# Performance work log

Measured on AMD Instinct MI355X. Metric: run time of the kernel, lower is better.

The kernel has to match this reference:

```python
import jax, jax.numpy as jnp
import numpy as np

EPS = 1e-12  # torch F.normalize eps


def _unfold(x, k, pad, stride):
    # torch F.unfold: [B,C,H,W] -> [B, C*k*k, L], channel-major then kernel (i,j)
    B, C, H, W = x.shape
    xp = jnp.pad(x, ((0, 0), (0, 0), (pad, pad), (pad, pad)))
    Ho = (H + 2 * pad - k) // stride + 1
    Wo = (W + 2 * pad - k) // stride + 1
    patches = [xp[:, :, i:i + stride * (Ho - 1) + 1:stride, j:j + stride * (Wo - 1) + 1:stride]
               for i in range(k) for j in range(k)]
    p = jnp.stack(patches, axis=2)  # [B, C, k*k, Ho, Wo]
    return p.reshape(B, C * k * k, Ho * Wo)


def _fold(t, out_hw, k, pad, stride):
    # torch F.fold: [B, C*k*k, L] -> [B, C, H, W] with overlap-add
    B, Ckk, L = t.shape
    C = Ckk // (k * k)
    H, W = out_hw
    Ho = (H + 2 * pad - k) // stride + 1
    Wo = (W + 2 * pad - k) // stride + 1
    t = t.reshape(B, C, k, k, Ho, Wo)
    out = jnp.zeros((B, C, H + 2 * pad, W + 2 * pad), t.dtype)
    for i in range(k):
        for j in range(k):
            out = out.at[:, :, i:i + stride * (Ho - 1) + 1:stride,
                         j:j + stride * (Wo - 1) + 1:stride].add(t[:, :, i, j])
    return out[:, :, pad:pad + H, pad:pad + W]


def setup_inputs() -> dict:
    key = jax.random.key(0)
    ks = jax.random.split(key, 5)
    B, C3, H3 = 4, 256, 48
    return {
        'dh_img_lv3': jax.random.normal(ks[0], (B, C3, H3, H3), jnp.float32),
        'dh_ref_lv3': jax.random.normal(ks[1], (B, C3, H3, H3), jnp.float32),
        'cl_ref_lv1': jax.random.normal(ks[2], (B, 64, H3 * 4, H3 * 4), jnp.float32),
        'cl_ref_lv2': jax.random.normal(ks[3], (B, 128, H3 * 2, H3 * 2), jnp.float32),
        'cl_ref_lv3': jax.random.normal(ks[4], (B, C3, H3, H3), jnp.float32),
    }


def reference(dh_img_lv3, dh_ref_lv3, cl_ref_lv1, cl_ref_lv2, cl_ref_lv3):
    ksz, pad = 3, 1
    B, C3, H3, W3 = dh_img_lv3.shape

    q = _unfold(dh_img_lv3, ksz, pad, 1)                      # [B, D, Lq]
    kmat = _unfold(dh_ref_lv3, ksz, pad, 1).transpose(0, 2, 1)  # [B, Lk, D]
    kmat = kmat / jnp.maximum(jnp.linalg.norm(kmat, axis=2, keepdims=True), EPS)
    q = q / jnp.maximum(jnp.linalg.norm(q, axis=1, keepdims=True), EPS)

    rel = jnp.einsum('bld,bdm->blm', kmat, q)                 # [B, Lk, Lq]
    rel_val = jnp.max(rel, axis=1, keepdims=True)             # [B, 1, Lq]  (top-1, k=1)
    rel_idx = jnp.argmax(rel, axis=1, keepdims=True)          # [B, 1, Lq]

    v3 = _unfold(cl_ref_lv3, ksz, pad, 1)                     # [B, C3*9,   Lk]
    v2 = _unfold(cl_ref_lv2, 2 * ksz, 2 * pad, 2)             # [B, C2*36,  Lk]
    v1 = _unfold(cl_ref_lv1, 4 * ksz, 4 * pad, 4)             # [B, C1*144, Lk]

    def transfer(v):
        idx = jnp.broadcast_to(rel_idx, (B, v.shape[1], rel_idx.shape[2]))
        tv = jnp.take_along_axis(v, idx, axis=2)              # [B, Cv, Lq]
        # weighted sum over k=1 topk / sum of weights (faithful to original)
        return (rel_val * tv) / rel_val

    T3u, T2u, T1u = transfer(v3), transfer(v2), transfer(v1)

    def fold_norm(Tu, scale, k_, p_, s_):
        hw = (H3 * scale, W3 * scale)
        cnt = _fold(jnp.ones_like(Tu), hw, k_, p_, s_)
        return _fold(Tu, hw, k_, p_, s_) / cnt

    T_lv3 = fold_norm(T3u, 1, ksz, pad, 1)
    T_lv2 = fold_norm(T2u, 2, 2 * ksz, 2 * pad, 2)
    T_lv1 = fold_norm(T1u, 4, 4 * ksz, 4 * pad, 4)

    S = rel_val.reshape(B, 1, H3, W3)
    return S, T_lv3, T_lv2, T_lv1
```

## Files before the change

### kernel.cpp

```cpp
#include <hip/hip_runtime.h>


#define HW3 2304
#define PLANE 589824
#define MP 2560
#define KP 512

typedef __bf16 v8bf __attribute__((ext_vector_type(8)));
typedef float v16f __attribute__((ext_vector_type(16)));

#define O_PSI  0
#define O_PSR  9216
#define O_IKN  18432
#define O_IQN  27648
#define O_RIDX 36864
#define O_IKNP 46080
#define O_CAND 56320
#define O_IMGT 74752
#define O_REFT 2434048
#define O_APL  4793344
#define O_BPL  7414784
#define O_S    10036224

__global__ __launch_bounds__(256) void k_pixsq(const float* __restrict__ img,
                                               const float* __restrict__ ref,
                                               float* __restrict__ psi,
                                               float* __restrict__ psr) {
  __shared__ float ri[16][17], rr[16][17];
  int t = threadIdx.x;
  int pl = t & 15, cg = t >> 4;
  int pix = blockIdx.x * 16 + pl;
  int b = pix / HW3, p = pix - b * HW3;
  const float* ib = img + (size_t)b * PLANE + p;
  const float* rb = ref + (size_t)b * PLANE + p;
  float si = 0.f, sr = 0.f;
#pragma unroll
  for (int c = 0; c < 16; ++c) {
    float x = ib[(cg * 16 + c) * HW3]; si = fmaf(x, x, si);
    float y = rb[(cg * 16 + c) * HW3]; sr = fmaf(y, y, sr);
  }
  ri[pl][cg] = si; rr[pl][cg] = sr;
  __syncthreads();
  if (t < 16) {
    float a = 0.f, s2 = 0.f;
#pragma unroll
    for (int g = 0; g < 16; ++g) { a += ri[t][g]; s2 += rr[t][g]; }
    int pix2 = blockIdx.x * 16 + t;
    psi[pix2] = a; psr[pix2] = s2;
  }
}

__global__ __launch_bounds__(256) void k_norm(const float* __restrict__ psr,
                                              const float* __restrict__ psi,
                                              float* __restrict__ ikn,
                                              float* __restrict__ iqn) {
  int pix = blockIdx.x * 256 + threadIdx.x;
  int b = pix / HW3, p = pix - b * HW3;
  int py = p / 48, px = p - py * 48;
  float sr = 0.f, si = 0.f;
#pragma unroll
  for (int dy = -1; dy <= 1; ++dy)
#pragma unroll
    for (int dx = -1; dx <= 1; ++dx) {
      if (py + dy < 0 || py + dy >= 48 || px + dx < 0 || px + dx >= 48) continue;
      int n = pix + dy * 48 + dx;
      sr += psr[n]; si += psi[n];
    }
  ikn[pix] = 1.0f / fmaxf(sqrtf(sr), 1e-12f);
  iqn[pix] = 1.0f / fmaxf(sqrtf(si), 1e-12f);
}

__global__ __launch_bounds__(256) void k_normp(const float* __restrict__ psr,
                                               float* __restrict__ iknp) {
  int idx = blockIdx.x * 256 + threadIdx.x;
  int b = idx / MP, pp = idx - b * MP;
  int py = pp / 50, px = pp - py * 50;
  float r = __uint_as_float(0x7fc00000u);
  if (pp < 2500 && py != 0 && py != 49 && px != 0 && px != 49) {
    int y = py - 1, x = px - 1;
    float s = 0.f;
    for (int dy = -1; dy <= 1; ++dy)
      for (int dx = -1; dx <= 1; ++dx) {
        int yy = y + dy, xx = x + dx;
        if (yy >= 0 && yy < 48 && xx >= 0 && xx < 48)
          s += psr[b * HW3 + yy * 48 + xx];
      }
    r = 1.0f / fmaxf(sqrtf(s), 1e-12f);
  }
  iknp[idx] = r;
}

__global__ __launch_bounds__(256) void k_padsplit(const float* __restrict__ src,
                                                  __bf16* __restrict__ dst) {
  __shared__ float sm[64][65];
  const int pix0 = blockIdx.x * 64, c0 = blockIdx.y * 64, b = blockIdx.z;
  const int lane = threadIdx.x & 63, q4 = threadIdx.x >> 6;
  const float* s = src + (size_t)b * PLANE;
#pragma unroll
  for (int r = 0; r < 16; ++r) {
    int cl = r * 4 + q4;
    sm[cl][lane] = s[(size_t)(c0 + cl) * HW3 + pix0 + lane];
  }
  __syncthreads();
  __bf16* d = dst + (size_t)b * MP * KP;
#pragma unroll
  for (int r = 0; r < 16; ++r) {
    int pl = r * 4 + q4;
    int p = pix0 + pl;
    int py = p / 48, px = p - py * 48;
    int pp = (py + 1) * 50 + px + 1;
    float v = sm[lane][pl];
    __bf16 hi = (__bf16)v;
    __bf16 lo = (__bf16)(v - (float)hi);
    d[(size_t)pp * KP + c0 + lane] = hi;
    d[(size_t)pp * KP + 256 + c0 + lane] = lo;
  }
}

__global__ __launch_bounds__(256) void k_tr(const float* __restrict__ src,
                                            float* __restrict__ dst,
                                            int C, int HW, int b0) {
  __shared__ float sm[64][65];
  int pix0 = blockIdx.x * 64, c0 = blockIdx.y * 64;
  const float* s = src + (size_t)(b0 + blockIdx.z) * C * HW;
  float* d = dst + (size_t)blockIdx.z * HW * C;
  int lane = threadIdx.x & 63, q4 = threadIdx.x >> 6;
#pragma unroll
  for (int r = 0; r < 16; ++r) {
    int cl = r * 4 + q4;
    sm[cl][lane] = s[(size_t)(c0 + cl) * HW + pix0 + lane];
  }
  __syncthreads();
#pragma unroll
  for (int r = 0; r < 16; ++r) {
    int pl = r * 4 + q4;
    d[(size_t)(pix0 + pl) * C + c0 + lane] = sm[lane][pl];
  }
}

__global__ __launch_bounds__(256) void k_gemm_mfma(const __bf16* __restrict__ Apl,
                                                   const __bf16* __restrict__ Bpl,
                                                   float* __restrict__ S, int b0) {
  __shared__ __bf16 As[128][72];
  __shared__ __bf16 Bs[128][72];
  const int b = b0 + blockIdx.z;
  const __bf16* Ab = Apl + (size_t)b * MP * KP;
  const __bf16* Bb = Bpl + (size_t)b * MP * KP;
  float* Sb = S + (size_t)blockIdx.z * (2560LL * 2560LL);
  const int t = threadIdx.x;
  const int q0 = blockIdx.y * 128, p0 = blockIdx.x * 128;
  const int lane = t & 63, w = t >> 6, wr = w >> 1, wc = w & 1;
  const int sr = t >> 1, ss = (t & 1) * 32;
  const int l31 = lane & 31, kb = (lane >> 5) * 8;

  v16f acc[2][2];
#pragma unroll
  for (int i = 0; i < 2; ++i)
#pragma unroll
    for (int j = 0; j < 2; ++j)
#pragma unroll
      for (int e = 0; e < 16; ++e) acc[i][j][e] = 0.f;

  for (int kv = 0; kv < 768; kv += 64) {
    const int ak = kv < 256 ? kv : kv - 256;
    const int bk = kv < 512 ? kv : kv - 512;
    const __bf16* ga = Ab + (size_t)(q0 + sr) * KP + ak + ss;
    const __bf16* gb = Bb + (size_t)(p0 + sr) * KP + bk + ss;
    float4 a0 = *(const float4*)(ga);
    float4 a1 = *(const float4*)(ga + 8);
    float4 a2 = *(const float4*)(ga + 16);
    float4 a3 = *(const float4*)(ga + 24);
    float4 b0v = *(const float4*)(gb);
    float4 b1v = *(const float4*)(gb + 8);
    float4 b2v = *(const float4*)(gb + 16);
    float4 b3v = *(const float4*)(gb + 24);
    __syncthreads();
    *(float4*)(&As[sr][ss])      = a0;
    *(float4*)(&As[sr][ss + 8])  = a1;
    *(float4*)(&As[sr][ss + 16]) = a2;
    *(float4*)(&As[sr][ss + 24]) = a3;
    *(float4*)(&Bs[sr][ss])      = b0v;
    *(float4*)(&Bs[sr][ss + 8])  = b1v;
    *(float4*)(&Bs[sr][ss + 16]) = b2v;
    *(float4*)(&Bs[sr][ss + 24]) = b3v;
    __syncthreads();
#pragma unroll
    for (int kk = 0; kk < 4; ++kk) {
      const int ko = kk * 16 + kb;
      v8bf af0 = *(const v8bf*)(&As[wr * 64 + l31][ko]);
      v8bf af1 = *(const v8bf*)(&As[wr * 64 + 32 + l31][ko]);
      v8bf bg0 = *(const v8bf*)(&Bs[wc * 64 + l31][ko]);
      v8bf bg1 = *(const v8bf*)(&Bs[wc * 64 + 32 + l31][ko]);
      acc[0][0] = __builtin_amdgcn_mfma_f32_32x32x16_bf16(af0, bg0, acc[0][0], 0, 0, 0);
      acc[0][1] = __builtin_amdgcn_mfma_f32_32x32x16_bf16(af0, bg1, acc[0][1], 0, 0, 0);
      acc[1][0] = __builtin_amdgcn_mfma_f32_32x32x16_bf16(af1, bg0, acc[1][0], 0, 0, 0);
      acc[1][1] = __builtin_amdgcn_mfma_f32_32x32x16_bf16(af1, bg1, acc[1][1], 0, 0, 0);
    }
  }
#pragma unroll
  for (int mf = 0; mf < 2; ++mf)
#pragma unroll
    for (int nf = 0; nf < 2; ++nf) {
      const int col = p0 + wc * 64 + nf * 32 + l31;
#pragma unroll
      for (int r = 0; r < 16; ++r) {
        const int row = q0 + wr * 64 + mf * 32 + (r & 3) + 8 * (r >> 2) + 4 * (lane >> 5);
        Sb[(size_t)row * MP + col] = acc[mf][nf][r];
      }
    }
}

__device__ __forceinline__ void top2merge(float& b1, int& i1, float& b2, int& i2,
                                          float o1, int oj1, float o2, int oj2) {
  if (o1 > b1 || (o1 == b1 && oj1 < i1)) {
    float t1 = b1; int tj = i1;
    b1 = o1; i1 = oj1;
    if (o2 > t1 || (o2 == t1 && oj2 < tj)) { b2 = o2; i2 = oj2; }
    else { b2 = t1; i2 = tj; }
  } else if (o1 > b2 || (o1 == b2 && oj1 < i2)) {
    b2 = o1; i2 = oj1;
  }
}

__global__ __launch_bounds__(256) void k_argmax_pad(const float* __restrict__ S,
                                                    const float* __restrict__ iknp,
                                                    int* __restrict__ cand, int b0) {
  __shared__ float L[30 * 258];
  __shared__ float smv[8][4][2];
  __shared__ int   smi[8][4][2];
  const int b = b0 + blockIdx.z;
  const float* Sb = S + (size_t)blockIdx.z * (2560LL * 2560LL);
  const float* ik = iknp + b * MP;
  const int qy = blockIdx.y, qx0 = blockIdx.x * 8;
  const int t = threadIdx.x, lane = t & 63, wv = t >> 6;
  const int gb[3] = { qy * 50 + qx0, (qy + 1) * 50 + qx0, (qy + 2) * 50 + qx0 };

  float b1[8], b2[8]; int i1[8], i2[8];
#pragma unroll
  for (int a = 0; a < 8; ++a) { b1[a] = -3e38f; b2[a] = -3e38f; i1[a] = 51; i2[a] = 51; }

  for (int pc = 0; pc < MP; pc += 256) {
    for (int row = wv; row < 30; row += 4) {
      int g = (row >= 20) ? 2 : (row >= 10 ? 1 : 0);
      int rr = row - g * 10;
      int gbase = (g == 0) ? gb[0] : (g == 1 ? gb[1] : gb[2]);
      int cb = pc + 50 * (g - 1) - 1;
      const float* src = Sb + (size_t)(gbase + rr) * MP;
      float* dstL = L + row * 258;
      for (int c = lane; c < 258; c += 64) {
        int cg = cb + c;
        float v = 0.f;
        if (cg >= 0 && cg < MP) v = src[cg];
        dstL[c] = v;
      }
    }
    __syncthreads();
    const float ikv = ik[pc + t];
    const int p = pc + t;
#pragma unroll
    for (int a = 0; a < 8; ++a) {
      float s = 0.f;
#pragma unroll
      for (int g = 0; g < 3; ++g)
#pragma unroll
        for (int dx = -1; dx <= 1; ++dx)
          s += L[(g * 10 + a + dx + 1) * 258 + (t + dx + 1)];
      float v = s * ikv;
      if (v > b1[a]) { b2[a] = b1[a]; i2[a] = i1[a]; b1[a] = v; i1[a] = p; }
      else if (v > b2[a]) { b2[a] = v; i2[a] = p; }
    }
    __syncthreads();
  }

#pragma unroll
  for (int a = 0; a < 8; ++a) {
    float x1 = b1[a], x2 = b2[a]; int j1 = i1[a], j2 = i2[a];
#pragma unroll
    for (int off = 32; off; off >>= 1) {
      float o1 = __shfl_down(x1, off), o2 = __shfl_down(x2, off);
      int oj1 = __shfl_down(j1, off), oj2 = __shfl_down(j2, off);
      top2merge(x1, j1, x2, j2, o1, oj1, o2, oj2);
    }
    if (lane == 0) { smv[a][wv][0] = x1; smv[a][wv][1] = x2; smi[a][wv][0] = j1; smi[a][wv][1] = j2; }
  }
  __syncthreads();
  if (t < 8) {
    float x1 = smv[t][0][0], x2 = smv[t][0][1]; int j1 = smi[t][0][0], j2 = smi[t][0][1];
#pragma unroll
    for (int w2 = 1; w2 < 4; ++w2)
      top2merge(x1, j1, x2, j2, smv[t][w2][0], smi[t][w2][0], smv[t][w2][1], smi[t][w2][1]);
    int q = qy * 48 + qx0 + t;
    cand[((size_t)b * HW3 + q) * 2]     = j1;
    cand[((size_t)b * HW3 + q) * 2 + 1] = j2;
  }
}

__global__ __launch_bounds__(256) void k_rescore(const float* __restrict__ imgT,
                                                 const float* __restrict__ refT,
                                                 const float* __restrict__ ikn,
                                                 const float* __restrict__ iqn,
                                                 const int* __restrict__ cand,
                                                 int* __restrict__ ridx,
                                                 float* __restrict__ outS) {
  const int t = threadIdx.x, lane = t & 63, sub = t >> 6;
  const int qg = blockIdx.x * 4 + sub;
  const int b = qg / HW3, q = qg - b * HW3;
  const int qy = q / 48, qx = q - qy * 48;
  const float* iT = imgT + (size_t)b * HW3 * 256;
  const float* rT = refT + (size_t)b * HW3 * 256;
  const int c0 = cand[qg * 2], c1 = cand[qg * 2 + 1];
  const int p0y = c0 / 50 - 1, p0x = c0 % 50 - 1;
  const int p1y = c1 / 50 - 1, p1x = c1 % 50 - 1;
  float s0 = 0.f, s1 = 0.f;
  for (int dy = -1; dy <= 1; ++dy) {
    int yq = qy + dy; if (yq < 0 || yq >= 48) continue;
    for (int dx = -1; dx <= 1; ++dx) {
      int xq = qx + dx; if (xq < 0 || xq >= 48) continue;
      const float* qrow = iT + (size_t)(yq * 48 + xq) * 256;
      int y0 = p0y + dy, x0 = p0x + dx;
      int y1 = p1y + dy, x1 = p1x + dx;
      bool v0 = (y0 >= 0 && y0 < 48 && x0 >= 0 && x0 < 48);
      bool v1 = (y1 >= 0 && y1 < 48 && x1 >= 0 && x1 < 48);
      const float* r0 = rT + (size_t)((v0 ? y0 * 48 + x0 : 0)) * 256;
      const float* r1 = rT + (size_t)((v1 ? y1 * 48 + x1 : 0)) * 256;
#pragma unroll
      for (int j = 0; j < 4; ++j) {
        float qv = qrow[lane + j * 64];
        if (v0) s0 = fmaf(qv, r0[lane + j * 64], s0);
        if (v1) s1 = fmaf(qv, r1[lane + j * 64], s1);
      }
    }
  }
#pragma unroll
  for (int off = 32; off; off >>= 1) {
    s0 += __shfl_down(s0, off);
    s1 += __shfl_down(s1, off);
  }
  if (lane == 0) {
    int m0 = p0y * 48 + p0x, m1 = p1y * 48 + p1x;
    float v0 = s0 * ikn[b * HW3 + m0], v1 = s1 * ikn[b * HW3 + m1];
    int win; float vw;
    if (v1 > v0 || (v1 == v0 && m1 < m0)) { win = m1; vw = v1; }
    else { win = m0; vw = v0; }
    ridx[b * HW3 + q] = win;
    outS[qg] = vw * iqn[b * HW3 + q];
  }
}

__global__ __launch_bounds__(256) void k_foldgather(const float* __restrict__ t,
                                                    const int* __restrict__ ridx,
                                                    float* __restrict__ out,
                                                    int C, int H, int sc, int b0) {
  __shared__ int   soff[64][9];
  __shared__ float sicnt[64];
  __shared__ float tr[64][65];
  const int HW = H * H;
  const int b = b0 + blockIdx.y;
  const float* tb = t + (size_t)blockIdx.y * HW * C;
  const int* rb = ridx + b * HW3;
  const int pix0 = blockIdx.x * 64;

  for (int e = threadIdx.x; e < 576; e += 256) {
    int op = e / 9, tap = e - op * 9;
    int pix = pix0 + op;
    int h = pix / H, w = pix - h * H;
    int hi = h / sc, hr = h - hi * sc;
    int wi = w / sc, wr = w - wi * sc;
    int ii = tap / 3, jj = tap - ii * 3;
    int oy = hi + 1 - ii, ox = wi + 1 - jj;
    int off = -1;
    if (oy >= 0 && oy < 48 && ox >= 0 && ox < 48) {
      int m = rb[oy * 48 + ox];
      int my = m / 48, mx = m - my * 48;
      int y = sc * (my - 1 + ii) + hr;
      int x = sc * (mx - 1 + jj) + wr;
      if (y >= 0 && y < H && x >= 0 && x < H) off = y * H + x;
    }
    soff[op][tap] = off;
    if (tap == 0) {
      int cnt = 0;
#pragma unroll
      for (int i2 = 0; i2 < 3; ++i2)
#pragma unroll
        for (int j2 = 0; j2 < 3; ++j2) {
          int oy2 = hi + 1 - i2, ox2 = wi + 1 - j2;
          if (oy2 >= 0 && oy2 < 48 && ox2 >= 0 && ox2 < 48) ++cnt;
        }
      sicnt[op] = 1.0f / (float)cnt;
    }
  }
  __syncthreads();

  const int g = threadIdx.x >> 6, lane = threadIdx.x & 63;
  for (int c0 = 0; c0 < C; c0 += 64) {
#pragma unroll
    for (int o = 0; o < 16; ++o) {
      int op = g * 16 + o;
      float s = 0.f;
#pragma unroll
      for (int tp = 0; tp < 9; ++tp) {
        int off = soff[op][tp];
        if (off >= 0) s += tb[(size_t)off * C + c0 + lane];
      }
      tr[op][lane] = s * sicnt[op];
    }
    __syncthreads();
#pragma unroll
    for (int r = 0; r < 16; ++r) {
      int cl = r * 4 + g;
      out[((size_t)b * C + c0 + cl) * HW + pix0 + lane] = tr[lane][cl];
    }
    __syncthreads();
  }
}

extern "C" void kernel_launch(void* const* d_in, const int* in_sizes, int n_in,
                              void* d_out, int out_size, void* d_ws, size_t ws_size,
                              hipStream_t stream) {
  (void)in_sizes; (void)n_in; (void)out_size;
  const float* img = (const float*)d_in[0];
  const float* ref = (const float*)d_in[1];
  const float* cl1 = (const float*)d_in[2];
  const float* cl2 = (const float*)d_in[3];
  const float* cl3 = (const float*)d_in[4];
  float* out = (float*)d_out;

  float* ws   = (float*)d_ws;
  float* ps_i = ws + O_PSI;
  float* ps_r = ws + O_PSR;
  float* ikn  = ws + O_IKN;
  float* iqn  = ws + O_IQN;
  int*   ridx = (int*)(ws + O_RIDX);
  float* iknp = ws + O_IKNP;
  int*   cand = (int*)(ws + O_CAND);
  float* imgT = ws + O_IMGT;
  float* refT = ws + O_REFT;
  __bf16* Apl = (__bf16*)(ws + O_APL);
  __bf16* Bpl = (__bf16*)(ws + O_BPL);
  float* Sm   = ws + O_S;

  hipMemsetAsync(ws + O_APL, 0, (size_t)(O_S - O_APL) * 4, stream);

  k_pixsq<<<576, 256, 0, stream>>>(img, ref, ps_i, ps_r);
  k_norm<<<36, 256, 0, stream>>>(ps_r, ps_i, ikn, iqn);
  k_normp<<<40, 256, 0, stream>>>(ps_r, iknp);
  k_padsplit<<<dim3(36, 4, 4), 256, 0, stream>>>(img, Apl);
  k_padsplit<<<dim3(36, 4, 4), 256, 0, stream>>>(ref, Bpl);
  k_tr<<<dim3(36, 4, 4), 256, 0, stream>>>(img, imgT, 256, HW3, 0);
  k_tr<<<dim3(36, 4, 4), 256, 0, stream>>>(ref, refT, 256, HW3, 0);

  const long long SPF = 2560LL * 2560LL;
  const long long availf = (long long)(ws_size / 4) - O_S;
  const int nb = (availf >= 4 * SPF) ? 4 : ((availf >= 2 * SPF) ? 2 : 1);
  for (int g = 0; g < 4; g += nb) {
    k_gemm_mfma<<<dim3(20, 20, nb), 256, 0, stream>>>(Apl, Bpl, Sm, g);
    k_argmax_pad<<<dim3(6, 48, nb), 256, 0, stream>>>(Sm, iknp, cand, g);
  }
  k_rescore<<<2304, 256, 0, stream>>>(imgT, refT, ikn, iqn, cand, ridx, out);

  float* t = ws + O_IMGT;
  k_tr<<<dim3(36, 4, 4), 256, 0, stream>>>(cl3, t, 256, 2304, 0);
  k_foldgather<<<dim3(36, 4), 256, 0, stream>>>(t, ridx, out + 9216, 256, 48, 1, 0);
  k_tr<<<dim3(144, 2, 4), 256, 0, stream>>>(cl2, t, 128, 9216, 0);
  k_foldgather<<<dim3(144, 4), 256, 0, stream>>>(t, ridx, out + 2368512, 128, 96, 2, 0);
  k_tr<<<dim3(576, 1, 4), 256, 0, stream>>>(cl1, t, 64, 36864, 0);
  k_foldgather<<<dim3(576, 4), 256, 0, stream>>>(t, ridx, out + 7087104, 64, 192, 4, 0);
}
```

Before: 800.2 us.

## Fuse diagonal x-tap summation into GEMM epilogue and skip fp32 rescoring when unambiguous

```diff
diff --git a/kernel.cpp b/kernel.cpp
--- a/kernel.cpp
+++ b/kernel.cpp
@@ -16,37 +16,35 @@
 #define O_RIDX 36864
 #define O_IKNP 46080
 #define O_CAND 56320
-#define O_IMGT 74752
-#define O_REFT 2434048
-#define O_APL  4793344
-#define O_BPL  7414784
-#define O_S    10036224
+#define O_CANDV 93184
+#define O_IMGT 130048
+#define O_REFT 2489344
+#define O_APL  4848640
+#define O_BPL  7470080
+#define O_U    10091520
 
 __global__ __launch_bounds__(256) void k_pixsq(const float* __restrict__ img,
                                                const float* __restrict__ ref,
                                                float* __restrict__ psi,
                                                float* __restrict__ psr) {
-  __shared__ float ri[16][17], rr[16][17];
-  int t = threadIdx.x;
-  int pl = t & 15, cg = t >> 4;
-  int pix = blockIdx.x * 16 + pl;
-  int b = pix / HW3, p = pix - b * HW3;
+  __shared__ float ri[4][64], rr[4][64];
+  const int t = threadIdx.x, lane = t & 63, cg = t >> 6;
+  const int pix = blockIdx.x * 64 + lane;
+  const int b = pix / HW3, p = pix - b * HW3;
   const float* ib = img + (size_t)b * PLANE + p;
   const float* rb = ref + (size_t)b * PLANE + p;
   float si = 0.f, sr = 0.f;
-#pragma unroll
-  for (int c = 0; c < 16; ++c) {
-    float x = ib[(cg * 16 + c) * HW3]; si = fmaf(x, x, si);
-    float y = rb[(cg * 16 + c) * HW3]; sr = fmaf(y, y, sr);
-  }
-  ri[pl][cg] = si; rr[pl][cg] = sr;
+#pragma unroll 8
+  for (int c = 0; c < 64; ++c) {
+    float x = ib[(cg * 64 + c) * HW3]; si = fmaf(x, x, si);
+    float y = rb[(cg * 64 + c) * HW3]; sr = fmaf(y, y, sr);
+  }
+  ri[cg][lane] = si; rr[cg][lane] = sr;
   __syncthreads();
-  if (t < 16) {
-    float a = 0.f, s2 = 0.f;
-#pragma unroll
-    for (int g = 0; g < 16; ++g) { a += ri[t][g]; s2 += rr[t][g]; }
-    int pix2 = blockIdx.x * 16 + t;
-    psi[pix2] = a; psr[pix2] = s2;
+  if (t < 64) {
+    float a = ri[0][t] + ri[1][t] + ri[2][t] + ri[3][t];
+    float s2 = rr[0][t] + rr[1][t] + rr[2][t] + rr[3][t];
+    psi[blockIdx.x * 64 + t] = a; psr[blockIdx.x * 64 + t] = s2;
   }
 }
 
@@ -138,20 +136,23 @@
   }
 }
 
-__global__ __launch_bounds__(256) void k_gemm_mfma(const __bf16* __restrict__ Apl,
-                                                   const __bf16* __restrict__ Bpl,
-                                                   float* __restrict__ S, int b0) {
-  __shared__ __bf16 As[128][72];
-  __shared__ __bf16 Bs[128][72];
+__global__ __launch_bounds__(256) void k_gemm_u(const __bf16* __restrict__ Apl,
+                                                const __bf16* __restrict__ Bpl,
+                                                float* __restrict__ U, int b0) {
+  __shared__ __align__(16) char smem[36864];
+  __bf16 (*As)[72] = (__bf16(*)[72])smem;
+  __bf16 (*Bs)[72] = (__bf16(*)[72])(smem + 18432);
   const int b = b0 + blockIdx.z;
   const __bf16* Ab = Apl + (size_t)b * MP * KP;
   const __bf16* Bb = Bpl + (size_t)b * MP * KP;
-  float* Sb = S + (size_t)blockIdx.z * (2560LL * 2560LL);
+  float* Ub = U + (size_t)blockIdx.z * (2560LL * 2560LL);
   const int t = threadIdx.x;
-  const int q0 = blockIdx.y * 128, p0 = blockIdx.x * 128;
+  const int q0 = blockIdx.y * 126 - 1, p0 = blockIdx.x * 126 - 1;
   const int lane = t & 63, w = t >> 6, wr = w >> 1, wc = w & 1;
   const int sr = t >> 1, ss = (t & 1) * 32;
   const int l31 = lane & 31, kb = (lane >> 5) * 8;
+  const int arow = q0 + sr, brow = p0 + sr;
+  const bool aok = (unsigned)arow < 2560u, bok = (unsigned)brow < 2560u;
 
   v16f acc[2][2];
 #pragma unroll
@@ -161,19 +162,20 @@
 #pragma unroll
       for (int e = 0; e < 16; ++e) acc[i][j][e] = 0.f;
 
+  const float4 z4 = make_float4(0.f, 0.f, 0.f, 0.f);
   for (int kv = 0; kv < 768; kv += 64) {
     const int ak = kv < 256 ? kv : kv - 256;
     const int bk = kv < 512 ? kv : kv - 512;
-    const __bf16* ga = Ab + (size_t)(q0 + sr) * KP + ak + ss;
-    const __bf16* gb = Bb + (size_t)(p0 + sr) * KP + bk + ss;
-    float4 a0 = *(const float4*)(ga);
-    float4 a1 = *(const float4*)(ga + 8);
-    float4 a2 = *(const float4*)(ga + 16);
-    float4 a3 = *(const float4*)(ga + 24);
-    float4 b0v = *(const float4*)(gb);
-    float4 b1v = *(const float4*)(gb + 8);
-    float4 b2v = *(const float4*)(gb + 16);
-    float4 b3v = *(const float4*)(gb + 24);
+    const __bf16* ga = Ab + (size_t)arow * KP + ak + ss;
+    const __bf16* gb = Bb + (size_t)brow * KP + bk + ss;
+    float4 a0 = aok ? *(const float4*)(ga)      : z4;
+    float4 a1 = aok ? *(const float4*)(ga + 8)  : z4;
+    float4 a2 = aok ? *(const float4*)(ga + 16) : z4;
+    float4 a3 = aok ? *(const float4*)(ga + 24) : z4;
+    float4 b0v = bok ? *(const float4*)(gb)      : z4;
+    float4 b1v = bok ? *(const float4*)(gb + 8)  : z4;
+    float4 b2v = bok ? *(const float4*)(gb + 16) : z4;
+    float4 b3v = bok ? *(const float4*)(gb + 24) : z4;
     __syncthreads();
     *(float4*)(&As[sr][ss])      = a0;
     *(float4*)(&As[sr][ss + 8])  = a1;
@@ -197,153 +199,185 @@
       acc[1][1] = __builtin_amdgcn_mfma_f32_32x32x16_bf16(af1, bg1, acc[1][1], 0, 0, 0);
     }
   }
-#pragma unroll
-  for (int mf = 0; mf < 2; ++mf)
-#pragma unroll
-    for (int nf = 0; nf < 2; ++nf) {
-      const int col = p0 + wc * 64 + nf * 32 + l31;
-#pragma unroll
-      for (int r = 0; r < 16; ++r) {
-        const int row = q0 + wr * 64 + mf * 32 + (r & 3) + 8 * (r >> 2) + 4 * (lane >> 5);
-        Sb[(size_t)row * MP + col] = acc[mf][nf][r];
+
+  float (*Sd)[128] = (float(*)[128])smem;
+#pragma unroll
+  for (int h = 0; h < 2; ++h) {
+    const int rlo = h * 63;
+    __syncthreads();
+#pragma unroll
+    for (int mf = 0; mf < 2; ++mf)
+#pragma unroll
+      for (int nf = 0; nf < 2; ++nf) {
+        const int col = wc * 64 + nf * 32 + l31;
+#pragma unroll
+        for (int r16 = 0; r16 < 16; ++r16) {
+          const int row = wr * 64 + mf * 32 + (r16 & 3) + 8 * (r16 >> 2) + 4 * (lane >> 5);
+          const int lr = row - rlo;
+          if (lr >= 0 && lr < 65) Sd[lr][col] = acc[mf][nf][r16];
+        }
       }
-    }
-}
-
-__device__ __forceinline__ void top2merge(float& b1, int& i1, float& b2, int& i2,
-                                          float o1, int oj1, float o2, int oj2) {
-  if (o1 > b1 || (o1 == b1 && oj1 < i1)) {
-    float t1 = b1; int tj = i1;
-    b1 = o1; i1 = oj1;
-    if (o2 > t1 || (o2 == t1 && oj2 < tj)) { b2 = o2; i2 = oj2; }
-    else { b2 = t1; i2 = tj; }
-  } else if (o1 > b2 || (o1 == b2 && oj1 < i2)) {
-    b2 = o1; i2 = oj1;
-  }
-}
-
-__global__ __launch_bounds__(256) void k_argmax_pad(const float* __restrict__ S,
-                                                    const float* __restrict__ iknp,
-                                                    int* __restrict__ cand, int b0) {
-  __shared__ float L[30 * 258];
-  __shared__ float smv[8][4][2];
-  __shared__ int   smi[8][4][2];
-  const int b = b0 + blockIdx.z;
-  const float* Sb = S + (size_t)blockIdx.z * (2560LL * 2560LL);
-  const float* ik = iknp + b * MP;
-  const int qy = blockIdx.y, qx0 = blockIdx.x * 8;
+    __syncthreads();
+    for (int idx = t; idx < 63 * 126; idx += 256) {
+      const int lr = idx / 126 + 1;
+      const int ce = idx - (lr - 1) * 126 + 1;
+      const int gq = q0 + rlo + lr;
+      const int gp = p0 + ce;
+      if ((unsigned)gq < 2560u && (unsigned)gp < 2560u)
+        Ub[(size_t)gq * 2560 + gp] = Sd[lr - 1][ce - 1] + Sd[lr][ce] + Sd[lr + 1][ce + 1];
+    }
+  }
+}
+
+__global__ __launch_bounds__(256) void k_argmax_u(const float* __restrict__ U,
+                                                  const float* __restrict__ iknp,
+                                                  int* __restrict__ cand,
+                                                  float* __restrict__ candv, int b0) {
+  __shared__ float Lu[24][356];
+  __shared__ float smv[16][4][2];
+  __shared__ int   smi[16][4][2];
+  const int zb = blockIdx.z >> 1, half = blockIdx.z & 1;
+  const int b = b0 + zb;
+  const float* Ub = U + (size_t)zb * (2560LL * 2560LL);
+  const int qy0 = blockIdx.y * 4, qx0 = blockIdx.x * 4;
+  const int kb = half * 1280;
   const int t = threadIdx.x, lane = t & 63, wv = t >> 6;
-  const int gb[3] = { qy * 50 + qx0, (qy + 1) * 50 + qx0, (qy + 2) * 50 + qx0 };
-
-  float b1[8], b2[8]; int i1[8], i2[8];
-#pragma unroll
-  for (int a = 0; a < 8; ++a) { b1[a] = -3e38f; b2[a] = -3e38f; i1[a] = 51; i2[a] = 51; }
-
-  for (int pc = 0; pc < MP; pc += 256) {
-    for (int row = wv; row < 30; row += 4) {
-      int g = (row >= 20) ? 2 : (row >= 10 ? 1 : 0);
-      int rr = row - g * 10;
-      int gbase = (g == 0) ? gb[0] : (g == 1 ? gb[1] : gb[2]);
-      int cb = pc + 50 * (g - 1) - 1;
-      const float* src = Sb + (size_t)(gbase + rr) * MP;
-      float* dstL = L + row * 258;
-      for (int c = lane; c < 258; c += 64) {
-        int cg = cb + c;
-        float v = 0.f;
-        if (cg >= 0 && cg < MP) v = src[cg];
-        dstL[c] = v;
+
+  float b1[16], b2[16]; int i1[16], i2[16];
+#pragma unroll
+  for (int i = 0; i < 16; ++i) { b1[i] = -3e38f; b2[i] = -3e38f; i1[i] = 0x3fffffff; i2[i] = 0x3fffffff; }
+
+  for (int ch = 0; ch < 5; ++ch) {
+    const int kc = kb + ch * 256;
+    for (int rr = wv; rr < 24; rr += 4) {
+      const int g = rr >> 2, a = rr & 3;
+      const float* src = Ub + (size_t)((qy0 + g) * 50 + qx0 + 1 + a) * 2560;
+      float* dst = Lu[rr];
+      for (int c = lane; c < 356; c += 64) {
+        const int gc = kc - 50 + c;
+        dst[c] = ((unsigned)gc < 2560u) ? src[gc] : 0.f;
       }
     }
     __syncthreads();
-    const float ikv = ik[pc + t];
-    const int p = pc + t;
-#pragma unroll
-    for (int a = 0; a < 8; ++a) {
-      float s = 0.f;
-#pragma unroll
-      for (int g = 0; g < 3; ++g)
-#pragma unroll
-        for (int dx = -1; dx <= 1; ++dx)
-          s += L[(g * 10 + a + dx + 1) * 258 + (t + dx + 1)];
-      float v = s * ikv;
-      if (v > b1[a]) { b2[a] = b1[a]; i2[a] = i1[a]; b1[a] = v; i1[a] = p; }
-      else if (v > b2[a]) { b2[a] = v; i2[a] = p; }
-    }
-    __syncthreads();
-  }
-
-#pragma unroll
-  for (int a = 0; a < 8; ++a) {
-    float x1 = b1[a], x2 = b2[a]; int j1 = i1[a], j2 = i2[a];
+    const float ikv = iknp[b * MP + kc + t];
+    const int p = kc + t;
+#pragma unroll
+    for (int e = 0; e < 4; ++e)
+#pragma unroll
+      for (int a = 0; a < 4; ++a) {
+        const float rel = Lu[e * 4 + a][t] + Lu[(e + 1) * 4 + a][t + 50] + Lu[(e + 2) * 4 + a][t + 100];
+        const float v = rel * ikv;
+        const int qi = e * 4 + a;
+        if (v > b1[qi]) { b2[qi] = b1[qi]; i2[qi] = i1[qi]; b1[qi] = v; i1[qi] = p; }
+        else if (v > b2[qi]) { b2[qi] = v; i2[qi] = p; }
+      }
+    __syncthreads();
+  }
+
+#pragma unroll
+  for (int qi = 0; qi < 16; ++qi) {
+    float x1 = b1[qi], x2 = b2[qi]; int j1 = i1[qi], j2 = i2[qi];
 #pragma unroll
     for (int off = 32; off; off >>= 1) {
       float o1 = __shfl_down(x1, off), o2 = __shfl_down(x2, off);
       int oj1 = __shfl_down(j1, off), oj2 = __shfl_down(j2, off);
-      top2merge(x1, j1, x2, j2, o1, oj1, o2, oj2);
-    }
-    if (lane == 0) { smv[a][wv][0] = x1; smv[a][wv][1] = x2; smi[a][wv][0] = j1; smi[a][wv][1] = j2; }
+      if (o1 > x1 || (o1 == x1 && oj1 < j1)) {
+        float tv = x1; int tj = j1;
+        x1 = o1; j1 = oj1;
+        if (o2 > tv || (o2 == tv && oj2 < tj)) { x2 = o2; j2 = oj2; }
+        else { x2 = tv; j2 = tj; }
+      } else if (o1 > x2 || (o1 == x2 && oj1 < j2)) { x2 = o1; j2 = oj1; }
+    }
+    if (lane == 0) { smv[qi][wv][0] = x1; smv[qi][wv][1] = x2; smi[qi][wv][0] = j1; smi[qi][wv][1] = j2; }
   }
   __syncthreads();
-  if (t < 8) {
+  if (t < 16) {
     float x1 = smv[t][0][0], x2 = smv[t][0][1]; int j1 = smi[t][0][0], j2 = smi[t][0][1];
 #pragma unroll
-    for (int w2 = 1; w2 < 4; ++w2)
-      top2merge(x1, j1, x2, j2, smv[t][w2][0], smi[t][w2][0], smv[t][w2][1], smi[t][w2][1]);
-    int q = qy * 48 + qx0 + t;
-    cand[((size_t)b * HW3 + q) * 2]     = j1;
-    cand[((size_t)b * HW3 + q) * 2 + 1] = j2;
-  }
-}
-
-__global__ __launch_bounds__(256) void k_rescore(const float* __restrict__ imgT,
-                                                 const float* __restrict__ refT,
-                                                 const float* __restrict__ ikn,
-                                                 const float* __restrict__ iqn,
-                                                 const int* __restrict__ cand,
-                                                 int* __restrict__ ridx,
-                                                 float* __restrict__ outS) {
-  const int t = threadIdx.x, lane = t & 63, sub = t >> 6;
-  const int qg = blockIdx.x * 4 + sub;
+    for (int w2 = 1; w2 < 4; ++w2) {
+      float o1 = smv[t][w2][0], o2 = smv[t][w2][1];
+      int oj1 = smi[t][w2][0], oj2 = smi[t][w2][1];
+      if (o1 > x1 || (o1 == x1 && oj1 < j1)) {
+        float tv = x1; int tj = j1;
+        x1 = o1; j1 = oj1;
+        if (o2 > tv || (o2 == tv && oj2 < tj)) { x2 = o2; j2 = oj2; }
+        else { x2 = tv; j2 = tj; }
+      } else if (o1 > x2 || (o1 == x2 && oj1 < j2)) { x2 = o1; j2 = oj1; }
+    }
+    int my1 = j1 / 50, my2 = j2 / 50;
+    int m1 = (my1 - 1) * 48 + (j1 - my1 * 50 - 1);
+    int m2 = (my2 - 1) * 48 + (j2 - my2 * 50 - 1);
+    const int q = (qy0 + (t >> 2)) * 48 + qx0 + (t & 3);
+    const size_t base = ((size_t)b * HW3 + q) * 4 + half * 2;
+    cand[base] = m1; cand[base + 1] = m2;
+    candv[base] = x1; candv[base + 1] = x2;
+  }
+}
+
+__global__ __launch_bounds__(256) void k_pick(const float* __restrict__ imgT,
+                                              const float* __restrict__ refT,
+                                              const float* __restrict__ ikn,
+                                              const float* __restrict__ iqn,
+                                              const int* __restrict__ cand,
+                                              const float* __restrict__ candv,
+                                              int* __restrict__ ridx,
+                                              float* __restrict__ outS) {
+  const int t = threadIdx.x, lane = t & 63, wv = t >> 6;
+  const int qg = blockIdx.x * 4 + wv;
   const int b = qg / HW3, q = qg - b * HW3;
-  const int qy = q / 48, qx = q - qy * 48;
-  const float* iT = imgT + (size_t)b * HW3 * 256;
-  const float* rT = refT + (size_t)b * HW3 * 256;
-  const int c0 = cand[qg * 2], c1 = cand[qg * 2 + 1];
-  const int p0y = c0 / 50 - 1, p0x = c0 % 50 - 1;
-  const int p1y = c1 / 50 - 1, p1x = c1 % 50 - 1;
-  float s0 = 0.f, s1 = 0.f;
-  for (int dy = -1; dy <= 1; ++dy) {
-    int yq = qy + dy; if (yq < 0 || yq >= 48) continue;
-    for (int dx = -1; dx <= 1; ++dx) {
-      int xq = qx + dx; if (xq < 0 || xq >= 48) continue;
-      const float* qrow = iT + (size_t)(yq * 48 + xq) * 256;
-      int y0 = p0y + dy, x0 = p0x + dx;
-      int y1 = p1y + dy, x1 = p1x + dx;
-      bool v0 = (y0 >= 0 && y0 < 48 && x0 >= 0 && x0 < 48);
-      bool v1 = (y1 >= 0 && y1 < 48 && x1 >= 0 && x1 < 48);
-      const float* r0 = rT + (size_t)((v0 ? y0 * 48 + x0 : 0)) * 256;
-      const float* r1 = rT + (size_t)((v1 ? y1 * 48 + x1 : 0)) * 256;
-#pragma unroll
-      for (int j = 0; j < 4; ++j) {
-        float qv = qrow[lane + j * 64];
-        if (v0) s0 = fmaf(qv, r0[lane + j * 64], s0);
-        if (v1) s1 = fmaf(qv, r1[lane + j * 64], s1);
+  int ci[4]; float cv[4];
+#pragma unroll
+  for (int s = 0; s < 4; ++s) { ci[s] = cand[(size_t)qg * 4 + s]; cv[s] = candv[(size_t)qg * 4 + s]; }
+  int o1 = 0;
+#pragma unroll
+  for (int s = 1; s < 4; ++s)
+    if (cv[s] > cv[o1] || (cv[s] == cv[o1] && ci[s] < ci[o1])) o1 = s;
+  int o2 = -1;
+#pragma unroll
+  for (int s = 0; s < 4; ++s) {
+    if (s == o1) continue;
+    if (o2 < 0 || cv[s] > cv[o2] || (cv[s] == cv[o2] && ci[s] < ci[o2])) o2 = s;
+  }
+  int m1 = ci[o1], m2 = ci[o2];
+  float v1 = cv[o1], v2 = cv[o2];
+  int win = m1; float wval = v1;
+  if (v1 - v2 <= 1e-5f * fmaxf(fabsf(v1), 1.0f)) {
+    const int qy = q / 48, qx = q - qy * 48;
+    const float* iT = imgT + (size_t)b * HW3 * 256;
+    const float* rT = refT + (size_t)b * HW3 * 256;
+    const int p1y = m1 / 48, p1x = m1 - p1y * 48;
+    const int p2y = m2 / 48, p2x = m2 - p2y * 48;
+    float s1 = 0.f, s2 = 0.f;
+    for (int dy = -1; dy <= 1; ++dy) {
+      int yq = qy + dy; if (yq < 0 || yq >= 48) continue;
+      for (int dx = -1; dx <= 1; ++dx) {
+        int xq = qx + dx; if (xq < 0 || xq >= 48) continue;
+        const float* qrow = iT + (size_t)(yq * 48 + xq) * 256;
+        int y1 = p1y + dy, x1 = p1x + dx, y2 = p2y + dy, x2 = p2x + dx;
+        bool k1 = (y1 >= 0 && y1 < 48 && x1 >= 0 && x1 < 48);
+        bool k2 = (y2 >= 0 && y2 < 48 && x2 >= 0 && x2 < 48);
+        const float* r1 = rT + (size_t)(k1 ? y1 * 48 + x1 : 0) * 256;
+        const float* r2 = rT + (size_t)(k2 ? y2 * 48 + x2 : 0) * 256;
+#pragma unroll
+        for (int j = 0; j < 4; ++j) {
+          float qv = qrow[lane + j * 64];
+          if (k1) s1 = fmaf(qv, r1[lane + j * 64], s1);
+          if (k2) s2 = fmaf(qv, r2[lane + j * 64], s2);
+        }
       }
     }
-  }
-#pragma unroll
-  for (int off = 32; off; off >>= 1) {
-    s0 += __shfl_down(s0, off);
-    s1 += __shfl_down(s1, off);
+#pragma unroll
+    for (int off = 32; off; off >>= 1) {
+      s1 += __shfl_down(s1, off);
+      s2 += __shfl_down(s2, off);
+    }
+    float e1 = s1 * ikn[b * HW3 + m1], e2 = s2 * ikn[b * HW3 + m2];
+    if (e2 > e1 || (e2 == e1 && m2 < m1)) { win = m2; wval = e2; }
+    else { win = m1; wval = e1; }
   }
   if (lane == 0) {
-    int m0 = p0y * 48 + p0x, m1 = p1y * 48 + p1x;
-    float v0 = s0 * ikn[b * HW3 + m0], v1 = s1 * ikn[b * HW3 + m1];
-    int win; float vw;
-    if (v1 > v0 || (v1 == v0 && m1 < m0)) { win = m1; vw = v1; }
-    else { win = m0; vw = v0; }
     ridx[b * HW3 + q] = win;
-    outS[qg] = vw * iqn[b * HW3 + q];
+    outS[qg] = wval * iqn[b * HW3 + q];
   }
 }
 
@@ -433,15 +467,16 @@
   int*   ridx = (int*)(ws + O_RIDX);
   float* iknp = ws + O_IKNP;
   int*   cand = (int*)(ws + O_CAND);
+  float* candv = ws + O_CANDV;
   float* imgT = ws + O_IMGT;
   float* refT = ws + O_REFT;
   __bf16* Apl = (__bf16*)(ws + O_APL);
   __bf16* Bpl = (__bf16*)(ws + O_BPL);
-  float* Sm   = ws + O_S;
-
-  hipMemsetAsync(ws + O_APL, 0, (size_t)(O_S - O_APL) * 4, stream);
-
-  k_pixsq<<<576, 256, 0, stream>>>(img, ref, ps_i, ps_r);
+  float* Um   = ws + O_U;
+
+  hipMemsetAsync(ws + O_APL, 0, (size_t)(O_U - O_APL) * 4, stream);
+
+  k_pixsq<<<144, 256, 0, stream>>>(img, ref, ps_i, ps_r);
   k_norm<<<36, 256, 0, stream>>>(ps_r, ps_i, ikn, iqn);
   k_normp<<<40, 256, 0, stream>>>(ps_r, iknp);
   k_padsplit<<<dim3(36, 4, 4), 256, 0, stream>>>(img, Apl);
@@ -449,14 +484,14 @@
   k_tr<<<dim3(36, 4, 4), 256, 0, stream>>>(img, imgT, 256, HW3, 0);
   k_tr<<<dim3(36, 4, 4), 256, 0, stream>>>(ref, refT, 256, HW3, 0);
 
-  const long long SPF = 2560LL * 2560LL;
-  const long long availf = (long long)(ws_size / 4) - O_S;
-  const int nb = (availf >= 4 * SPF) ? 4 : ((availf >= 2 * SPF) ? 2 : 1);
+  const long long UPF = 2560LL * 2560LL;
+  const long long availf = (long long)(ws_size / 4) - O_U;
+  const int nb = (availf >= 4 * UPF) ? 4 : ((availf >= 2 * UPF) ? 2 : 1);
   for (int g = 0; g < 4; g += nb) {
-    k_gemm_mfma<<<dim3(20, 20, nb), 256, 0, stream>>>(Apl, Bpl, Sm, g);
-    k_argmax_pad<<<dim3(6, 48, nb), 256, 0, stream>>>(Sm, iknp, cand, g);
-  }
-  k_rescore<<<2304, 256, 0, stream>>>(imgT, refT, ikn, iqn, cand, ridx, out);
+    k_gemm_u<<<dim3(21, 21, nb), 256, 0, stream>>>(Apl, Bpl, Um, g);
+    k_argmax_u<<<dim3(12, 12, nb * 2), 256, 0, stream>>>(Um, iknp, cand, candv, g);
+  }
+  k_pick<<<2304, 256, 0, stream>>>(imgT, refT, ikn, iqn, cand, candv, ridx, out);
 
   float* t = ws + O_IMGT;
   k_tr<<<dim3(36, 4, 4), 256, 0, stream>>>(cl3, t, 256, 2304, 0);
```

After: 885.8 us. 1.11x slower.
